# Kernel tuning notes

Measured on AMD Instinct MI355X. Metric: run time of the kernel, lower is better.

## Reference

```python
import jax, jax.numpy as jnp
import numpy as np

N = 65536      # total nodes (ground + sub)
NG = 32768     # ground nodes (subnodes are NG..N)
H = 64         # n_hidden
FIN = 32       # n_node_features
L = 2          # num_convolution_blocks
B = 64         # graphs in batch
MAXDEG = 10    # MFConv max_degree -> 11 buckets
EG = 1048576   # ground-graph edges
ES = 1048576   # subgraph edges
EX = 524288    # cross (ground<->sub) edges


def setup_inputs() -> dict:
    key = jax.random.key(0)
    ks = jax.random.split(key, 32)
    NS = N - NG
    x = jax.random.normal(ks[0], (N, FIN), jnp.float32)
    # ground graph: src/dst in [0, NG)
    edge_index = jax.random.randint(ks[1], (2, EG), 0, NG).astype(jnp.int64)
    # subgraph: src/dst in [NG, N)
    subgraph_edge_index = (NG + jax.random.randint(ks[2], (2, ES), 0, NS)).astype(jnp.int64)
    # ground -> sub
    ns_src = jax.random.randint(ks[3], (EX,), 0, NG)
    ns_dst = NG + jax.random.randint(ks[4], (EX,), 0, NS)
    node_subnode_index = jnp.stack([ns_src, ns_dst]).astype(jnp.int64)
    # sub -> ground
    sn_src = NG + jax.random.randint(ks[5], (EX,), 0, NS)
    sn_dst = jax.random.randint(ks[6], (EX,), 0, NG)
    subnode_node_index = jnp.stack([sn_src, sn_dst]).astype(jnp.int64)
    ground_node = jnp.arange(N) < NG
    subgraph_batch_index = jax.random.randint(ks[7], (N,), 0, B).astype(jnp.int64)
    batch_idx = jax.random.randint(ks[8], (N,), 0, B).astype(jnp.int64)
    s = 0.05
    p = {}
    p['embed_W'] = jax.random.normal(ks[9], (FIN, H), jnp.float32) * s
    p['embed_b'] = jnp.zeros((H,), jnp.float32)
    names = ['ground', 'g2s', 'sub', 's2g']
    for i, nm in enumerate(names):
        p[nm + '_Wl'] = jax.random.normal(ks[10 + 3 * i], (L, MAXDEG + 1, H, H), jnp.float32) * s
        p[nm + '_bl'] = jnp.zeros((L, MAXDEG + 1, H), jnp.float32)
        p[nm + '_Wr'] = jax.random.normal(ks[11 + 3 * i], (L, MAXDEG + 1, H, H), jnp.float32) * s
    p['W1'] = jax.random.normal(ks[24], (H, H), jnp.float32) * s
    p['b1'] = jnp.zeros((H,), jnp.float32)
    p['W2'] = jax.random.normal(ks[25], (H, 1), jnp.float32) * s
    p['b2'] = jnp.zeros((1,), jnp.float32)
    return dict(x=x, edge_index=edge_index, subgraph_edge_index=subgraph_edge_index,
                node_subnode_index=node_subnode_index, subnode_node_index=subnode_node_index,
                ground_node=ground_node, subgraph_batch_index=subgraph_batch_index,
                batch_idx=batch_idx, **p)


def _mfconv(h, src, dst, Wl, bl, Wr):
    # PyG MFConv: out_i = Lin_l[deg_i](sum_{j->i} h_j) + Lin_r[deg_i](h_i), deg clamped to MAXDEG
    n = h.shape[0]
    deg = jnp.clip(jax.ops.segment_sum(jnp.ones(src.shape[0], jnp.int32), dst, num_segments=n), 0, MAXDEG)
    agg = jax.ops.segment_sum(h[src], dst, num_segments=n)  # [n, H] sum aggregation
    out = jnp.zeros((n, Wl.shape[-1]), h.dtype)
    for d in range(MAXDEG + 1):
        m = (deg == d)[:, None]
        out = out + jnp.where(m, agg @ Wl[d] + bl[d] + h @ Wr[d], jnp.zeros((), h.dtype))
    return out


def _masked_conv(h, ei, Wl, bl, Wr):
    # nodes that never receive a message keep their old features (catch_lone_sender)
    src, dst = ei[0], ei[1]
    recv = jnp.zeros((h.shape[0],), bool).at[dst].set(True)
    return jnp.where(recv[:, None], _mfconv(h, src, dst, Wl, bl, Wr), h)


def reference(x, edge_index, subgraph_edge_index, node_subnode_index, subnode_node_index,
              ground_node, subgraph_batch_index, batch_idx,
              embed_W, embed_b,
              ground_Wl, ground_bl, ground_Wr,
              g2s_Wl, g2s_bl, g2s_Wr,
              sub_Wl, sub_bl, sub_Wr,
              s2g_Wl, s2g_bl, s2g_Wr,
              W1, b1, W2, b2):
    h = x @ embed_W + embed_b
    for l in range(L):
        if l > 0:
            h = jax.nn.relu(h)
        h = _masked_conv(h, edge_index, ground_Wl[l], ground_bl[l], ground_Wr[l])
        h = _masked_conv(h, node_subnode_index, g2s_Wl[l], g2s_bl[l], g2s_Wr[l])
        h = _masked_conv(h, subgraph_edge_index, sub_Wl[l], sub_bl[l], sub_Wr[l])
        h = _masked_conv(h, subnode_node_index, s2g_Wl[l], s2g_bl[l], s2g_Wr[l])
    # global_add_pool over ground nodes only
    pooled = jax.ops.segment_sum(jnp.where(ground_node[:, None], h, jnp.zeros((), h.dtype)),
                                 batch_idx, num_segments=B)  # [B, H]
    z = jax.nn.relu(pooled @ W1 + b1)
    return z @ W2 + b2  # [B, 1]
```

## Files before the change

kernel.cpp:

```cpp
#include <hip/hip_runtime.h>

#define N_NODES 65536
#define NGROUND 32768
#define NHALF 32768
#define H 64
#define FIN 32
#define NB 64
#define MAXDEG 10
#define RSTRIDE 32769
#define EG 1048576
#define ES 1048576
#define EX 524288
#define TE (EG + EX + ES + EX)
#define BIN2 512
#define NPB 64
#define CHUNK 8192
#define TC 384
#define CNT_LEN 196608
#define NSCANB 192
#define BCAP 6144
#define NEB 2048
#define NFB 32

typedef __attribute__((ext_vector_type(8))) short short8;
typedef __attribute__((ext_vector_type(4))) float f32x4;
typedef __attribute__((ext_vector_type(2))) unsigned int u32x2;
typedef __attribute__((ext_vector_type(4))) unsigned int u32x4;
typedef unsigned short u16;
typedef unsigned int u32;

__device__ __forceinline__ u16 f2bf(float x) {
    unsigned int u = __float_as_uint(x);
    unsigned int r = u + 0x7FFFu + ((u >> 16) & 1u);
    return (u16)(r >> 16);
}
__device__ __forceinline__ float bf2f(u16 b) {
    return __uint_as_float(((unsigned int)b) << 16);
}
__device__ __forceinline__ u32 relu2(u32 w) {
    u32 lo = w & 0xFFFFu;
    if (lo & 0x8000u) lo = 0;
    u32 hi = w >> 16;
    if (hi & 0x8000u) hi = 0;
    return lo | (hi << 16);
}

__device__ __forceinline__ void chunk_resolve(int b, int& set, int& cin,
                                              int& nc, int& base, int& dbase, int& sbase) {
    if (b < 128)      { set = 0; cin = b;       nc = 128; base = 0;      dbase = 0;       sbase = 0; }
    else if (b < 192) { set = 1; cin = b - 128; nc = 64;  base = 65536;  dbase = NGROUND; sbase = 0; }
    else if (b < 320) { set = 2; cin = b - 192; nc = 128; base = 98304;  dbase = NGROUND; sbase = NGROUND; }
    else              { set = 3; cin = b - 320; nc = 64;  base = 163840; dbase = 0;       sbase = NGROUND; }
}

__global__ __launch_bounds__(256) void embed_prep_count_kernel(
    const float* __restrict__ x, const float* __restrict__ W,
    const float* __restrict__ b, u16* __restrict__ hgHi, u16* __restrict__ hsHi,
    const float* W0l, const float* W0r, const float* W1l, const float* W1r,
    const float* W2l, const float* W2r, const float* W3l, const float* W3r,
    short8* __restrict__ fragbuf,
    const int* __restrict__ d0, const int* __restrict__ d1,
    const int* __restrict__ d2, const int* __restrict__ d3,
    int* __restrict__ cnt) {
    int tid = threadIdx.x;
    if (blockIdx.x >= NEB + NFB) {
        __shared__ int hist[BIN2];
        int set, cin, nc, base, dbase, sbase;
        chunk_resolve(blockIdx.x - NEB - NFB, set, cin, nc, base, dbase, sbase);
        const int* dp = set == 0 ? d0 : set == 1 ? d1 : set == 2 ? d2 : d3;
        for (int i = tid; i < BIN2; i += 256) hist[i] = 0;
        __syncthreads();
        int e0 = cin * CHUNK;
        for (int i = tid; i < CHUNK; i += 256) {
            int d = __builtin_nontemporal_load(&dp[e0 + i]) - dbase;
            atomicAdd(&hist[d >> 6], 1);
        }
        __syncthreads();
        for (int i = tid; i < BIN2; i += 256)
            cnt[base + i * nc + cin] = hist[i];
        return;
    }
    if (blockIdx.x >= NEB) {
        int tid2 = (blockIdx.x - NEB) * 256 + tid;
        int lane = tid2 & 63;
        int f8 = (tid2 >> 6) & 7;
        int mat = (tid2 >> 9) & 1;
        int layer = (tid2 >> 10) & 1;
        int set = (tid2 >> 11) & 3;
        int s = f8 >> 2, t = f8 & 3;
        const float* Wb;
        if (set == 0) Wb = mat ? W0r : W0l;
        else if (set == 1) Wb = mat ? W1r : W1l;
        else if (set == 2) Wb = mat ? W2r : W2l;
        else Wb = mat ? W3r : W3l;
        Wb += ((size_t)layer * (MAXDEG + 1) + MAXDEG) * H * H;
        int k0 = s * 32 + (lane >> 4) * 8;
        int n = t * 16 + (lane & 15);
        short8 hi, lo;
#pragma unroll
        for (int j = 0; j < 8; j++) {
            float w = Wb[(size_t)(k0 + j) * H + n];
            u16 hb = f2bf(w);
            u16 lb = f2bf(w - bf2f(hb));
            hi[j] = (short)hb;
            lo[j] = (short)lb;
        }
        size_t basehi = ((size_t)(((set * 2 + layer) * 2 + mat) * 2 + 0) * 8 + f8) * 64 + lane;
        size_t baselo = ((size_t)(((set * 2 + layer) * 2 + mat) * 2 + 1) * 8 + f8) * 64 + lane;
        fragbuf[basehi] = hi;
        fragbuf[baselo] = lo;
        return;
    }
    int f = tid & 63;
    int wy = tid >> 6;
    __shared__ float sW[FIN * H];
    for (int i = tid; i < FIN * H; i += 256) sW[i] = W[i];
    __syncthreads();
    float bf_ = b[f];
#pragma unroll
    for (int it = 0; it < 8; it++) {
        int node = blockIdx.x * 32 + it * 4 + wy;
        const float* xr = x + (size_t)node * FIN;
        float acc = bf_;
#pragma unroll
        for (int k = 0; k < FIN; k++) acc += xr[k] * sW[k * H + f];
        if (node < NGROUND)
            hgHi[(size_t)node * H + f] = f2bf(acc);
        else
            hsHi[(size_t)(node - NGROUND) * H + f] = f2bf(acc);
    }
}

__global__ __launch_bounds__(256) void scanA_kernel(
    int* __restrict__ cnt, int* __restrict__ bsum) {
    __shared__ int lds[256];
    int t = threadIdx.x;
    int base = blockIdx.x * 1024 + t * 4;
    int v0 = cnt[base], v1 = cnt[base + 1], v2 = cnt[base + 2], v3 = cnt[base + 3];
    int s = v0 + v1 + v2 + v3;
    lds[t] = s;
    __syncthreads();
    for (int d = 1; d < 256; d <<= 1) {
        int x = 0;
        if (t >= d) x = lds[t - d];
        __syncthreads();
        lds[t] += x;
        __syncthreads();
    }
    int pref = lds[t] - s;
    cnt[base] = pref;
    cnt[base + 1] = pref + v0;
    cnt[base + 2] = pref + v0 + v1;
    cnt[base + 3] = pref + v0 + v1 + v2;
    if (t == 255) bsum[blockIdx.x] = pref + s;
}

__global__ __launch_bounds__(256) void scanB_kernel(int* __restrict__ bsum) {
    __shared__ int lds[256];
    int t = threadIdx.x;
    int v = (t < NSCANB) ? bsum[t] : 0;
    lds[t] = v;
    __syncthreads();
    for (int d = 1; d < 256; d <<= 1) {
        int x = 0;
        if (t >= d) x = lds[t - d];
        __syncthreads();
        lds[t] += x;
        __syncthreads();
    }
    if (t < NSCANB) bsum[t] = lds[t] - v;
}

__global__ __launch_bounds__(256) void partition_kernel(
    const int* __restrict__ s0, const int* __restrict__ s1,
    const int* __restrict__ s2, const int* __restrict__ s3,
    const int* __restrict__ d0, const int* __restrict__ d1,
    const int* __restrict__ d2, const int* __restrict__ d3,
    const int* __restrict__ cnt, const int* __restrict__ bsum,
    u32* __restrict__ csru) {
    __shared__ u32 buf[CHUNK];
    __shared__ int hist[BIN2];
    __shared__ int lofs[BIN2];
    __shared__ int gbase[BIN2];
    __shared__ int sc[256];
    int set, cin, nc, base, dbase, sbase;
    chunk_resolve(blockIdx.x, set, cin, nc, base, dbase, sbase);
    const int* dp = set == 0 ? d0 : set == 1 ? d1 : set == 2 ? d2 : d3;
    const int* sp = set == 0 ? s0 : set == 1 ? s1 : set == 2 ? s2 : s3;
    int t = threadIdx.x;
    for (int i = t; i < BIN2; i += 256) hist[i] = 0;
    __syncthreads();
    u32 pk[32];
    int e0 = cin * CHUNK;
#pragma unroll
    for (int j = 0; j < 32; j++) {
        int idx = e0 + t + j * 256;
        int d = __builtin_nontemporal_load(&dp[idx]) - dbase;
        int s = __builtin_nontemporal_load(&sp[idx]) - sbase;
        pk[j] = ((u32)d << 15) | (u32)s;
        atomicAdd(&hist[d >> 6], 1);
    }
    __syncthreads();
    int h0 = hist[2 * t], h1 = hist[2 * t + 1];
    int hs = h0 + h1;
    sc[t] = hs;
    __syncthreads();
    for (int d2 = 1; d2 < 256; d2 <<= 1) {
        int v = 0;
        if (t >= d2) v = sc[t - d2];
        __syncthreads();
        sc[t] += v;
        __syncthreads();
    }
    int pref = sc[t] - hs;
    lofs[2 * t] = pref;
    lofs[2 * t + 1] = pref + h0;
    hist[2 * t] = pref;
    hist[2 * t + 1] = pref + h0;
    for (int i = t; i < BIN2; i += 256) {
        int idx = base + i * nc + cin;
        gbase[i] = cnt[idx] + bsum[idx >> 10];
    }
    __syncthreads();
#pragma unroll
    for (int j = 0; j < 32; j++) {
        int bin = pk[j] >> 21;
        int pos = atomicAdd(&hist[bin], 1);
        buf[pos] = pk[j];
    }
    __syncthreads();
    for (int i = t; i < CHUNK; i += 256) {
        u32 pkt = buf[i];
        int d = pkt >> 15;
        int bin = d >> 6;
        int gpos = gbase[bin] + (i - lofs[bin]);
        csru[gpos] = pkt & 0x1FFFFFu;
    }
}

__global__ __launch_bounds__(256) void finalize_kernel(
    u32* __restrict__ csru, const int* __restrict__ cnt,
    const int* __restrict__ bsum, int* __restrict__ rowstart4) {
    __shared__ u32 buf[BCAP];
    __shared__ int deg[NPB], off[NPB];
    int b = blockIdx.x;
    int set = b >> 9, bin = b & 511;
    int nc = (set == 0 || set == 2) ? 128 : 64;
    int base = set == 0 ? 0 : set == 1 ? 65536 : set == 2 ? 98304 : 163840;
    int flat = base + bin * nc;
    int binstart = cnt[flat] + bsum[flat >> 10];
    int binend = (b == 2047) ? TE : (cnt[flat + nc] + bsum[(flat + nc) >> 10]);
    int n = binend - binstart;
    for (int i = threadIdx.x; i < n; i += 256) buf[i] = csru[binstart + i];
    if (threadIdx.x < NPB) deg[threadIdx.x] = 0;
    __syncthreads();
    for (int i = threadIdx.x; i < n; i += 256) atomicAdd(&deg[buf[i] >> 15], 1);
    __syncthreads();
    if (threadIdx.x == 0) {
        int r = 0;
        for (int j = 0; j < NPB; j++) { off[j] = r; r += deg[j]; }
    }
    __syncthreads();
    int coffset = set == 0 ? 0 : set == 1 ? EG : set == 2 ? EG + EX : EG + EX + ES;
    if (threadIdx.x < NPB)
        rowstart4[set * RSTRIDE + bin * NPB + threadIdx.x] =
            binstart - coffset + off[threadIdx.x];
    if (bin == 0 && threadIdx.x == 0)
        rowstart4[set * RSTRIDE + NHALF] = (set == 0 || set == 2) ? EG : EX;
    if (threadIdx.x < NPB) deg[threadIdx.x] = off[threadIdx.x];
    __syncthreads();
    for (int i = threadIdx.x; i < n; i += 256) {
        u32 pkt = buf[i];
        int dl = pkt >> 15;
        int pos = atomicAdd(&deg[dl], 1);
        csru[binstart + pos] = pkt & 0x7FFFu;
    }
}

__global__ __launch_bounds__(256, 8) void conv_fused_kernel(
    const u16* __restrict__ srcHi, const u16* __restrict__ selfHi,
    u16* __restrict__ outHi, const int* __restrict__ csr,
    const int* __restrict__ rowstart, const short8* __restrict__ fragbase,
    const float* __restrict__ Wlp, const float* __restrict__ Wrp,
    const float* __restrict__ blp, int do_relu, u32* __restrict__ relu_buf) {
    if (blockIdx.x >= 2048) {
        int base = ((blockIdx.x - 2048) * 256 + threadIdx.x) * 2;
        u32x4* p = (u32x4*)relu_buf;
        u32x4 a = p[base], b = p[base + 1];
        a.x = relu2(a.x); a.y = relu2(a.y); a.z = relu2(a.z); a.w = relu2(a.w);
        b.x = relu2(b.x); b.y = relu2(b.y); b.z = relu2(b.z); b.w = relu2(b.w);
        p[base] = a;
        p[base + 1] = b;
        return;
    }
    __shared__ __align__(16) char smem[4 * 128 * 16 * 2];
    u16 (*sB)[128][16] = (u16 (*)[128][16])smem;
    float (*sAgg)[68] = (float (*)[68])smem;
    int tid = threadIdx.x;
    int w = tid >> 6, lane = tid & 63;
    int node0 = blockIdx.x * 16;
    int q = lane >> 4, mrow = lane & 15;

    int R0 = rowstart[node0];
    int R16 = rowstart[node0 + 16];
    int rlo = rowstart[node0 + mrow];
    int rhi = rowstart[node0 + mrow + 1];
    u32 rspan = (u32)(rhi - rlo);
    R16 = min(max(R16, R0), R0 + 8192);

    f32x4 aggv = (f32x4){0.f, 0.f, 0.f, 0.f};

    int p_ = lane & 7;
    int eb = w * 32 + (lane >> 3);
    u32 lds_rd = (u32)(uintptr_t)(&sB[w][0][0]) + (u32)lane * 8u;

    for (int ce = R0; ce < R16; ce += 128) {
        int s0 = csr[min(ce + eb,      R16 - 1)];
        int s1 = csr[min(ce + eb + 8,  R16 - 1)];
        int s2 = csr[min(ce + eb + 16, R16 - 1)];
        int s3 = csr[min(ce + eb + 24, R16 - 1)];
        u32x4 v0 = *((const u32x4*)(srcHi + (size_t)s0 * H) + p_);
        u32x4 v1 = *((const u32x4*)(srcHi + (size_t)s1 * H) + p_);
        u32x4 v2 = *((const u32x4*)(srcHi + (size_t)s2 * H) + p_);
        u32x4 v3 = *((const u32x4*)(srcHi + (size_t)s3 * H) + p_);
        __syncthreads();
        *(u32x4*)&sB[p_ >> 1][eb][(p_ & 1) * 8] = v0;
        *(u32x4*)&sB[p_ >> 1][eb + 8][(p_ & 1) * 8] = v1;
        *(u32x4*)&sB[p_ >> 1][eb + 16][(p_ & 1) * 8] = v2;
        *(u32x4*)&sB[p_ >> 1][eb + 24][(p_ & 1) * 8] = v3;
        __syncthreads();
        u32x2 r0, r1, r2, r3, r4, r5, r6, r7;
        asm volatile(
            "ds_read_b64_tr_b16 %0, %8 offset:0\n\t"
            "ds_read_b64_tr_b16 %1, %8 offset:512\n\t"
            "ds_read_b64_tr_b16 %2, %8 offset:1024\n\t"
            "ds_read_b64_tr_b16 %3, %8 offset:1536\n\t"
            "ds_read_b64_tr_b16 %4, %8 offset:2048\n\t"
            "ds_read_b64_tr_b16 %5, %8 offset:2560\n\t"
            "ds_read_b64_tr_b16 %6, %8 offset:3072\n\t"
            "ds_read_b64_tr_b16 %7, %8 offset:3584\n\t"
            "s_waitcnt lgkmcnt(0)"
            : "=&v"(r0), "=&v"(r1), "=&v"(r2), "=&v"(r3),
              "=&v"(r4), "=&v"(r5), "=&v"(r6), "=&v"(r7)
            : "v"(lds_rd)
            : "memory");
        __builtin_amdgcn_sched_barrier(0);
#pragma unroll
        for (int half = 0; half < 4; half++) {
            int ebase = ce + half * 32 + q * 4;
            short8 Af;
#pragma unroll
            for (int j = 0; j < 8; j++) {
                int E = ebase + ((j < 4) ? j : (12 + j));
                u32 off = (u32)E - (u32)rlo;
                Af[j] = (off < rspan) ? (short)0x3F80 : (short)0;
            }
            union { short8 s; u32 u[4]; } bb;
            u32x2 ra = (half == 0) ? r0 : (half == 1) ? r2 : (half == 2) ? r4 : r6;
            u32x2 rb = (half == 0) ? r1 : (half == 1) ? r3 : (half == 2) ? r5 : r7;
            bb.u[0] = ra[0]; bb.u[1] = ra[1];
            bb.u[2] = rb[0]; bb.u[3] = rb[1];
            aggv = __builtin_amdgcn_mfma_f32_16x16x32_bf16(Af, bb.s, aggv, 0, 0, 0);
        }
    }
    __syncthreads();
#pragma unroll
    for (int r = 0; r < 4; r++) sAgg[q * 4 + r][w * 16 + mrow] = aggv[r];
    __syncthreads();

    int myrow = node0 + mrow;
    int mydeg = rhi - rlo;
    unsigned long long ball = __ballot(min(mydeg, MAXDEG) != MAXDEG);
    unsigned exc = (unsigned)(ball & 0xFFFFull);
    int t = w;

    f32x4 accv = (f32x4){0.f, 0.f, 0.f, 0.f};
    const short8* fb = fragbase + lane;
#pragma unroll
    for (int s = 0; s < 2; s++) {
        float av[8];
        *(float4*)&av[0] = *(const float4*)&sAgg[mrow][s * 32 + q * 8];
        *(float4*)&av[4] = *(const float4*)&sAgg[mrow][s * 32 + q * 8 + 4];
        short8 Ahi;
#pragma unroll
        for (int j = 0; j < 8; j++) Ahi[j] = (short)f2bf(av[j]);
        short8 Hhi = *(const short8*)(selfHi + (size_t)myrow * H + s * 32 + q * 8);
        short8 BLhi = fb[(size_t)((0 * 8) + s * 4 + t) * 64];
        short8 BLlo = fb[(size_t)((1 * 8) + s * 4 + t) * 64];
        short8 BRhi = fb[(size_t)((2 * 8) + s * 4 + t) * 64];
        short8 BRlo = fb[(size_t)((3 * 8) + s * 4 + t) * 64];
        accv = __builtin_amdgcn_mfma_f32_16x16x32_bf16(Ahi, BLhi, accv, 0, 0, 0);
        accv = __builtin_amdgcn_mfma_f32_16x16x32_bf16(Ahi, BLlo, accv, 0, 0, 0);
        accv = __builtin_amdgcn_mfma_f32_16x16x32_bf16(Hhi, BRhi, accv, 0, 0, 0);
        accv = __builtin_amdgcn_mfma_f32_16x16x32_bf16(Hhi, BRlo, accv, 0, 0, 0);
    }

    {
        int n = t * 16 + mrow;
        float bv = blp[MAXDEG * H + n];
#pragma unroll
        for (int r = 0; r < 4; r++) {
            int mm = q * 4 + r;
            if (!((exc >> mm) & 1)) {
                float val = accv[r] + bv;
                if (do_relu) val = fmaxf(val, 0.f);
                outHi[(size_t)(node0 + mm) * H + n] = f2bf(val);
            }
        }
    }

    if (exc & (0xFu << (w * 4))) {
        for (int i = 0; i < 4; i++) {
            int nr = w * 4 + i;
            if (!((exc >> nr) & 1)) continue;
            int node = node0 + nr;
            int st = rowstart[node], en = rowstart[node + 1];
            int dg = en - st;
            if (dg == 0) {
                float v = bf2f(selfHi[(size_t)node * H + lane]);
                if (do_relu) v = fmaxf(v, 0.f);
                outHi[(size_t)node * H + lane] = f2bf(v);
            } else {
                int d = min(dg, MAXDEG);
                const float* wl = Wlp + (size_t)d * H * H;
                const float* wr = Wrp + (size_t)d * H * H;
                float sval = bf2f(selfHi[(size_t)node * H + lane]);
                float o = blp[d * H + lane];
#pragma unroll 4
                for (int k = 0; k < H; k++) {
                    o += sAgg[nr][k] * wl[k * H + lane];
                    o += __shfl(sval, k, 64) * wr[k * H + lane];
                }
                if (do_relu) o = fmaxf(o, 0.f);
                outHi[(size_t)node * H + lane] = f2bf(o);
            }
        }
    }
}

__global__ __launch_bounds__(256) void pool_kernel(
    const u16* __restrict__ hgHi, const int* __restrict__ batch_idx,
    float* __restrict__ pooled) {
    __shared__ float lp[NB * H];
    int tid = threadIdx.x;
    for (int i = tid; i < NB * H; i += 256) lp[i] = 0.f;
    __syncthreads();
    int f = tid & 63;
    int wave = tid >> 6;
    int start = blockIdx.x * 64;
    for (int n = wave; n < 64; n += 4) {
        int node = start + n;
        int bi = batch_idx[node];
        atomicAdd(&lp[bi * H + f], bf2f(hgHi[(size_t)node * H + f]));
    }
    __syncthreads();
    for (int i = tid; i < NB * H; i += 256) {
        float v = lp[i];
        if (v != 0.f) atomicAdd(&pooled[i], v);
    }
}

__global__ __launch_bounds__(64) void mlp_kernel(
    const float* __restrict__ pooled, const float* __restrict__ W1,
    const float* __restrict__ b1, const float* __restrict__ W2,
    const float* __restrict__ b2, float* __restrict__ out) {
    int b = blockIdx.x;
    int j = threadIdx.x;
    const float* pr = pooled + b * H;
    float acc = b1[j];
#pragma unroll
    for (int k = 0; k < H; k++) acc += pr[k] * W1[k * H + j];
    acc = fmaxf(acc, 0.f);
    float v = acc * W2[j];
#pragma unroll
    for (int off = 32; off > 0; off >>= 1) v += __shfl_down(v, off, 64);
    if (j == 0) out[b] = v + b2[0];
}

extern "C" void kernel_launch(void* const* d_in, const int* in_sizes, int n_in,
                              void* d_out, int out_size, void* d_ws, size_t ws_size,
                              hipStream_t stream) {
    const float* x = (const float*)d_in[0];
    const int* ei_ground = (const int*)d_in[1];
    const int* ei_sub = (const int*)d_in[2];
    const int* ei_g2s = (const int*)d_in[3];
    const int* ei_s2g = (const int*)d_in[4];
    const int* batch_idx = (const int*)d_in[7];
    const float* embed_W = (const float*)d_in[8];
    const float* embed_b = (const float*)d_in[9];
    const float* Wl[4] = {(const float*)d_in[10], (const float*)d_in[13],
                          (const float*)d_in[16], (const float*)d_in[19]};
    const float* bl[4] = {(const float*)d_in[11], (const float*)d_in[14],
                          (const float*)d_in[17], (const float*)d_in[20]};
    const float* Wr[4] = {(const float*)d_in[12], (const float*)d_in[15],
                          (const float*)d_in[18], (const float*)d_in[21]};
    const float* W1 = (const float*)d_in[22];
    const float* b1 = (const float*)d_in[23];
    const float* W2 = (const float*)d_in[24];
    const float* b2 = (const float*)d_in[25];

    const int* s_[4] = {ei_ground, ei_g2s, ei_sub, ei_s2g};
    const int* dsr[4] = {ei_ground + EG, ei_g2s + EX, ei_sub + ES, ei_s2g + EX};
    const size_t coff[4] = {0, (size_t)EG, (size_t)EG + EX, (size_t)EG + EX + ES};

    const size_t HB = (size_t)NHALF * H * sizeof(u16);
    char* p = (char*)d_ws;
    u16* hgHi[2] = {(u16*)p, (u16*)(p + HB)};            p += 2 * HB;
    u16* hsHi[2] = {(u16*)p, (u16*)(p + HB)};            p += 2 * HB;
    u32* csru = (u32*)p;           p += (size_t)TE * sizeof(u32);
    int* cnt = (int*)p;            p += (size_t)CNT_LEN * sizeof(int);
    int* bsum = (int*)p;           p += (size_t)NSCANB * sizeof(int);
    int* rowstart4 = (int*)p;      p += (size_t)4 * RSTRIDE * sizeof(int);
    p += 16 - ((size_t)p & 15);
    short8* fragbuf = (short8*)p;  p += (size_t)8192 * sizeof(short8);
    float* pooled = (float*)p;

    embed_prep_count_kernel<<<NEB + NFB + TC, 256, 0, stream>>>(
        x, embed_W, embed_b, hgHi[0], hsHi[0],
        Wl[0], Wr[0], Wl[1], Wr[1], Wl[2], Wr[2], Wl[3], Wr[3], fragbuf,
        dsr[0], dsr[1], dsr[2], dsr[3], cnt);

    scanA_kernel<<<NSCANB, 256, 0, stream>>>(cnt, bsum);
    scanB_kernel<<<1, 256, 0, stream>>>(bsum);
    partition_kernel<<<TC, 256, 0, stream>>>(
        s_[0], s_[1], s_[2], s_[3], dsr[0], dsr[1], dsr[2], dsr[3], cnt, bsum, csru);
    finalize_kernel<<<2048, 256, 0, stream>>>(csru, cnt, bsum, rowstart4);
    const int* csr = (const int*)csru;

    int cg = 0, cs = 0;
    for (int l = 0; l < 2; l++) {
        for (int c = 0; c < 4; c++) {
            const u16 *srcHi, *selfHi;
            u16 *outHi;
            if (c == 0)      { srcHi = hgHi[cg]; selfHi = hgHi[cg]; outHi = hgHi[1 - cg]; }
            else if (c == 1) { srcHi = hgHi[cg]; selfHi = hsHi[cs]; outHi = hsHi[1 - cs]; }
            else if (c == 2) { srcHi = hsHi[cs]; selfHi = hsHi[cs]; outHi = hsHi[1 - cs]; }
            else             { srcHi = hsHi[cs]; selfHi = hgHi[cg]; outHi = hgHi[1 - cg]; }
            int do_relu = (l == 0 && c == 3) ? 1 : 0;
            int relu_blocks = (l == 1 && c == 0) ? 512 : 0;
            u32* relu_buf = (l == 1 && c == 0) ? (u32*)hsHi[cs] : (u32*)nullptr;
            conv_fused_kernel<<<2048 + relu_blocks, 256, 0, stream>>>(
                srcHi, selfHi, outHi,
                csr + coff[c], rowstart4 + (size_t)c * RSTRIDE,
                fragbuf + (size_t)(c * 2 + l) * 2048,
                Wl[c] + (size_t)l * (MAXDEG + 1) * H * H,
                Wr[c] + (size_t)l * (MAXDEG + 1) * H * H,
                bl[c] + (size_t)l * (MAXDEG + 1) * H, do_relu, relu_buf);
            if (c == 0 || c == 3) cg ^= 1; else cs ^= 1;
        }
    }

    hipMemsetAsync(pooled, 0, (size_t)NB * H * sizeof(float), stream);
    pool_kernel<<<NGROUND / 64, 256, 0, stream>>>(hgHi[cg], batch_idx, pooled);
    mlp_kernel<<<NB, 64, 0, stream>>>(pooled, W1, b1, W2, b2, (float*)d_out);
}
```

Baseline: 379.5 us.

## Give each wave a private edge-slice LDS tile and reduce partial aggregates after

Restructures the gather-aggregate loop so each wave loads and transposes its own 32-edge slice into a private, padded LDS region, with no block-wide barriers per 128-edge chunk. Each wave now accumulates all 64 feature columns in four MFMA accumulators, and the four wave partials are summed through shared memory after the loop. The LDS rows are padded (stride 1056) to reduce bank conflicts on the transposed reads. In exchange it uses more LDS and registers, drops the occupancy hint from launch bounds, and adds a cross-wave reduction pass.

```diff
diff --git a/kernel.cpp b/kernel.cpp
--- a/kernel.cpp
+++ b/kernel.cpp
@@ -21,6 +21,9 @@
 #define BCAP 6144
 #define NEB 2048
 #define NFB 32
+#define QSTR 1056
+#define WSTR (4 * QSTR)
+#define SMEMSZ 17408
 
 typedef __attribute__((ext_vector_type(8))) short short8;
 typedef __attribute__((ext_vector_type(4))) float f32x4;
@@ -277,7 +280,7 @@
     }
 }
 
-__global__ __launch_bounds__(256, 8) void conv_fused_kernel(
+__global__ __launch_bounds__(256) void conv_fused_kernel(
     const u16* __restrict__ srcHi, const u16* __restrict__ selfHi,
     u16* __restrict__ outHi, const int* __restrict__ csr,
     const int* __restrict__ rowstart, const short8* __restrict__ fragbase,
@@ -293,9 +296,8 @@
         p[base + 1] = b;
         return;
     }
-    __shared__ __align__(16) char smem[4 * 128 * 16 * 2];
-    u16 (*sB)[128][16] = (u16 (*)[128][16])smem;
-    float (*sAgg)[68] = (float (*)[68])smem;
+    __shared__ __align__(16) char smem[SMEMSZ];
+    float* smemF = (float*)smem;
     int tid = threadIdx.x;
     int w = tid >> 6, lane = tid & 63;
     int node0 = blockIdx.x * 16;
@@ -308,65 +310,84 @@
     u32 rspan = (u32)(rhi - rlo);
     R16 = min(max(R16, R0), R0 + 8192);
 
-    f32x4 aggv = (f32x4){0.f, 0.f, 0.f, 0.f};
+    f32x4 agg0 = (f32x4){0.f, 0.f, 0.f, 0.f};
+    f32x4 agg1 = (f32x4){0.f, 0.f, 0.f, 0.f};
+    f32x4 agg2 = (f32x4){0.f, 0.f, 0.f, 0.f};
+    f32x4 agg3 = (f32x4){0.f, 0.f, 0.f, 0.f};
 
     int p_ = lane & 7;
-    int eb = w * 32 + (lane >> 3);
-    u32 lds_rd = (u32)(uintptr_t)(&sB[w][0][0]) + (u32)lane * 8u;
+    int er = lane >> 3;
+    u32 wbase = (u32)w * WSTR;
+    u32 wr_base = wbase + (u32)(p_ >> 1) * QSTR + (u32)(p_ & 1) * 16u;
+    u32 rd_base = wbase + (u32)lane * 8u;
 
     for (int ce = R0; ce < R16; ce += 128) {
-        int s0 = csr[min(ce + eb,      R16 - 1)];
-        int s1 = csr[min(ce + eb + 8,  R16 - 1)];
-        int s2 = csr[min(ce + eb + 16, R16 - 1)];
-        int s3 = csr[min(ce + eb + 24, R16 - 1)];
+        int eb = ce + w * 32;
+        int s0 = csr[min(eb + er,      R16 - 1)];
+        int s1 = csr[min(eb + er + 8,  R16 - 1)];
+        int s2 = csr[min(eb + er + 16, R16 - 1)];
+        int s3 = csr[min(eb + er + 24, R16 - 1)];
         u32x4 v0 = *((const u32x4*)(srcHi + (size_t)s0 * H) + p_);
         u32x4 v1 = *((const u32x4*)(srcHi + (size_t)s1 * H) + p_);
         u32x4 v2 = *((const u32x4*)(srcHi + (size_t)s2 * H) + p_);
         u32x4 v3 = *((const u32x4*)(srcHi + (size_t)s3 * H) + p_);
-        __syncthreads();
-        *(u32x4*)&sB[p_ >> 1][eb][(p_ & 1) * 8] = v0;
-        *(u32x4*)&sB[p_ >> 1][eb + 8][(p_ & 1) * 8] = v1;
-        *(u32x4*)&sB[p_ >> 1][eb + 16][(p_ & 1) * 8] = v2;
-        *(u32x4*)&sB[p_ >> 1][eb + 24][(p_ & 1) * 8] = v3;
-        __syncthreads();
+        *(u32x4*)(smem + wr_base + (u32)er * 32u)         = v0;
+        *(u32x4*)(smem + wr_base + (u32)(er + 8) * 32u)   = v1;
+        *(u32x4*)(smem + wr_base + (u32)(er + 16) * 32u)  = v2;
+        *(u32x4*)(smem + wr_base + (u32)(er + 24) * 32u)  = v3;
         u32x2 r0, r1, r2, r3, r4, r5, r6, r7;
         asm volatile(
             "ds_read_b64_tr_b16 %0, %8 offset:0\n\t"
             "ds_read_b64_tr_b16 %1, %8 offset:512\n\t"
-            "ds_read_b64_tr_b16 %2, %8 offset:1024\n\t"
-            "ds_read_b64_tr_b16 %3, %8 offset:1536\n\t"
-            "ds_read_b64_tr_b16 %4, %8 offset:2048\n\t"
-            "ds_read_b64_tr_b16 %5, %8 offset:2560\n\t"
-            "ds_read_b64_tr_b16 %6, %8 offset:3072\n\t"
-            "ds_read_b64_tr_b16 %7, %8 offset:3584\n\t"
+            "ds_read_b64_tr_b16 %2, %8 offset:1056\n\t"
+            "ds_read_b64_tr_b16 %3, %8 offset:1568\n\t"
+            "ds_read_b64_tr_b16 %4, %8 offset:2112\n\t"
+            "ds_read_b64_tr_b16 %5, %8 offset:2624\n\t"
+            "ds_read_b64_tr_b16 %6, %8 offset:3168\n\t"
+            "ds_read_b64_tr_b16 %7, %8 offset:3680\n\t"
             "s_waitcnt lgkmcnt(0)"
             : "=&v"(r0), "=&v"(r1), "=&v"(r2), "=&v"(r3),
               "=&v"(r4), "=&v"(r5), "=&v"(r6), "=&v"(r7)
-            : "v"(lds_rd)
+            : "v"(rd_base)
             : "memory");
         __builtin_amdgcn_sched_barrier(0);
-#pragma unroll
-        for (int half = 0; half < 4; half++) {
-            int ebase = ce + half * 32 + q * 4;
-            short8 Af;
-#pragma unroll
-            for (int j = 0; j < 8; j++) {
-                int E = ebase + ((j < 4) ? j : (12 + j));
-                u32 off = (u32)E - (u32)rlo;
-                Af[j] = (off < rspan) ? (short)0x3F80 : (short)0;
-            }
-            union { short8 s; u32 u[4]; } bb;
-            u32x2 ra = (half == 0) ? r0 : (half == 1) ? r2 : (half == 2) ? r4 : r6;
-            u32x2 rb = (half == 0) ? r1 : (half == 1) ? r3 : (half == 2) ? r5 : r7;
-            bb.u[0] = ra[0]; bb.u[1] = ra[1];
-            bb.u[2] = rb[0]; bb.u[3] = rb[1];
-            aggv = __builtin_amdgcn_mfma_f32_16x16x32_bf16(Af, bb.s, aggv, 0, 0, 0);
-        }
-    }
-    __syncthreads();
-#pragma unroll
-    for (int r = 0; r < 4; r++) sAgg[q * 4 + r][w * 16 + mrow] = aggv[r];
-    __syncthreads();
+        short8 Af;
+#pragma unroll
+        for (int j = 0; j < 8; j++) {
+            int E = eb + q * 4 + ((j < 4) ? j : (12 + j));
+            u32 off = (u32)E - (u32)rlo;
+            Af[j] = (off < rspan) ? (short)0x3F80 : (short)0;
+        }
+        union { short8 s; u32 u[4]; } b0, b1, b2, b3;
+        b0.u[0] = r0[0]; b0.u[1] = r0[1]; b0.u[2] = r1[0]; b0.u[3] = r1[1];
+        b1.u[0] = r2[0]; b1.u[1] = r2[1]; b1.u[2] = r3[0]; b1.u[3] = r3[1];
+        b2.u[0] = r4[0]; b2.u[1] = r4[1]; b2.u[2] = r5[0]; b2.u[3] = r5[1];
+        b3.u[0] = r6[0]; b3.u[1] = r6[1]; b3.u[2] = r7[0]; b3.u[3] = r7[1];
+        agg0 = __builtin_amdgcn_mfma_f32_16x16x32_bf16(Af, b0.s, agg0, 0, 0, 0);
+        agg1 = __builtin_amdgcn_mfma_f32_16x16x32_bf16(Af, b1.s, agg1, 0, 0, 0);
+        agg2 = __builtin_amdgcn_mfma_f32_16x16x32_bf16(Af, b2.s, agg2, 0, 0, 0);
+        agg3 = __builtin_amdgcn_mfma_f32_16x16x32_bf16(Af, b3.s, agg3, 0, 0, 0);
+    }
+    __syncthreads();
+    {
+        float* pw = smemF + (size_t)w * 1088;
+#pragma unroll
+        for (int r = 0; r < 4; r++) {
+            int rowoff = (q * 4 + r) * 68;
+            pw[rowoff + 0 * 16 + mrow] = agg0[r];
+            pw[rowoff + 1 * 16 + mrow] = agg1[r];
+            pw[rowoff + 2 * 16 + mrow] = agg2[r];
+            pw[rowoff + 3 * 16 + mrow] = agg3[r];
+        }
+    }
+    __syncthreads();
+    for (int i = tid; i < 1024; i += 256) {
+        int r = i >> 6, c = i & 63;
+        int o = r * 68 + c;
+        smemF[o] += smemF[1088 + o] + smemF[2176 + o] + smemF[3264 + o];
+    }
+    __syncthreads();
+    float (*sAgg)[68] = (float (*)[68])smemF;
 
     int myrow = node0 + mrow;
     int mydeg = rhi - rlo;
```

New measurement: 386.8 us. No clear change (+1.9%).
